# Performance work log

Hardware: AMD Instinct MI355X
Metric: run time of the kernel (lower is better)

Reference implementation:

```python
import jax, jax.numpy as jnp
import numpy as np

B, S, H, DH = 8, 1024, 16, 64
D = H * DH  # d_model = 1024
M_ALPHA = -1e9


def setup_inputs() -> dict:
    key = jax.random.key(0)
    ks = jax.random.split(key, 11)
    scale = 1.0 / np.sqrt(D)
    x = jax.random.normal(ks[0], (B, S, D), dtype=jnp.float32)
    # 0/1 padding mask, shape [B, S, 1] (1 = masked position)
    mask = (jax.random.uniform(ks[1], (B, S, 1)) < 0.25).astype(jnp.float32)
    mk = lambda k: jax.random.normal(k, (D, D), dtype=jnp.float32) * scale
    return {
        "x": x,
        "mask": mask,
        "wq_w": mk(ks[2]), "wq_b": jnp.zeros((D,), jnp.float32),
        "wk_w": mk(ks[3]), "wk_b": jnp.zeros((D,), jnp.float32),
        "wv_w": mk(ks[4]), "wv_b": jnp.zeros((D,), jnp.float32),
        "wo_w": mk(ks[5]), "wo_b": jnp.zeros((D,), jnp.float32),
    }


def _split_heads(t):
    # [B, S, D] -> [B, H, S, DH]
    return t.reshape(B, S, H, DH).transpose(0, 2, 1, 3)


def reference(x, mask, wq_w, wq_b, wk_w, wk_b, wv_w, wv_b, wo_w, wo_b):
    q = _split_heads(x @ wq_w + wq_b)  # [B,H,S,DH]
    k = _split_heads(x @ wk_w + wk_b)
    v = _split_heads(x @ wv_w + wv_b)

    logits = jnp.einsum("bhqd,bhkd->bhqk", q, k) / jnp.sqrt(
        jnp.asarray(DH, jnp.float32))
    qk_values = logits  # pre-mask scaled logits (temperature == 0.0 -> no-op)

    # QK mask path: mask [B,S,1] -> tile to [B,S,S] rows (m[b,i,j] = mask[b,i]),
    # then symmetrize (square) -> mask[b,i] + mask[b,j], clamp at 1.
    m = mask[:, :, 0]                               # [B,S]
    mask_qk = jnp.minimum(1.0, m[:, :, None] + m[:, None, :])  # [B,S,S]
    logits = logits + mask_qk[:, None, :, :] * M_ALPHA

    attn = jax.nn.softmax(logits, axis=-1)          # [B,H,S,S]
    z = jnp.einsum("bhqk,bhkd->bhqd", attn, v)      # [B,H,S,DH]
    z = z.transpose(0, 2, 1, 3).reshape(B, S, D)
    out = z @ wo_w + wo_b
    return (out, attn, qk_values, q, k, v)
```

## Files before the change

kernel.cpp:

```cpp
#include <hip/hip_runtime.h>
#include <hip/hip_bf16.h>
#include <stdint.h>

#define BB 8
#define SS 1024
#define HH 16
#define DHD 64
#define DD 1024

typedef __attribute__((ext_vector_type(8))) short bf16x8;
typedef __attribute__((ext_vector_type(4))) float f32x4;

__device__ __forceinline__ unsigned short f2bf(float f) {
  unsigned u = __builtin_bit_cast(unsigned, f);
  u += 0x7fffu + ((u >> 16) & 1u);
  return (unsigned short)(u >> 16);
}

__device__ __forceinline__ unsigned swz(unsigned a) { return a ^ ((a >> 3) & 0x70u); }

#define GLOAD16(gp, lp)                                                        \
  __builtin_amdgcn_global_load_lds(                                            \
      (const __attribute__((address_space(1))) unsigned int*)(gp),             \
      (__attribute__((address_space(3))) unsigned int*)(lp), 16, 0, 0)

#define MFMA16(a, b, c) __builtin_amdgcn_mfma_f32_16x16x32_bf16(a, b, c, 0, 0, 0)

__global__ __launch_bounds__(256) void cvt_x_kernel(const float* __restrict__ x,
                                                    unsigned short* __restrict__ xb) {
  int i = blockIdx.x * 256 + threadIdx.x;
  float4 v = ((const float4*)x)[i];
  ushort4 o;
  o.x = f2bf(v.x); o.y = f2bf(v.y); o.z = f2bf(v.z); o.w = f2bf(v.w);
  ((ushort4*)xb)[i] = o;
}

__global__ __launch_bounds__(256) void transpose_w_kernel(
    const float* __restrict__ w0, const float* __restrict__ w1,
    const float* __restrict__ w2, const float* __restrict__ w3,
    unsigned short* __restrict__ o0, unsigned short* __restrict__ o1,
    unsigned short* __restrict__ o2, unsigned short* __restrict__ o3) {
  __shared__ float tile[32][33];
  const float* src; unsigned short* dst;
  if (blockIdx.z == 0)      { src = w0; dst = o0; }
  else if (blockIdx.z == 1) { src = w1; dst = o1; }
  else if (blockIdx.z == 2) { src = w2; dst = o2; }
  else                      { src = w3; dst = o3; }
  int n0 = blockIdx.x * 32, k0 = blockIdx.y * 32;
  int tx = threadIdx.x, ty = threadIdx.y;
#pragma unroll
  for (int j = 0; j < 32; j += 8)
    tile[ty + j][tx] = src[(size_t)(k0 + ty + j) * DD + n0 + tx];
  __syncthreads();
#pragma unroll
  for (int j = 0; j < 32; j += 8)
    dst[(size_t)(n0 + ty + j) * DD + k0 + tx] = f2bf(tile[tx][ty + j]);
}

__global__ __launch_bounds__(256) void proj_gemm_kernel(
    const unsigned short* __restrict__ xb,
    const unsigned short* __restrict__ wqt, const unsigned short* __restrict__ wkt,
    const unsigned short* __restrict__ wvt,
    const float* __restrict__ bq, const float* __restrict__ bk, const float* __restrict__ bv,
    float* __restrict__ qo, float* __restrict__ ko, float* __restrict__ vo,
    unsigned short* __restrict__ qb, unsigned short* __restrict__ kbf,
    unsigned short* __restrict__ vt) {
  __shared__ __align__(128) unsigned short smem[2 * 128 * 64];
  unsigned short* As = smem;
  unsigned short* Bs = smem + 128 * 64;
  const int tid = threadIdx.x, lane = tid & 63, w = tid >> 6;
  const int wr = (w >> 1) * 64, wc = (w & 1) * 64;
  const int m0 = blockIdx.x * 128;
  const int mat = blockIdx.y >> 3;
  const int n0 = (blockIdx.y & 7) * 128;
  const unsigned short* Bg = (mat == 0) ? wqt : (mat == 1) ? wkt : wvt;
  const float* bias = (mat == 0) ? bq : (mat == 1) ? bk : bv;

  f32x4 acc[4][4];
  f32x4 z4 = {0.f, 0.f, 0.f, 0.f};
#pragma unroll
  for (int i = 0; i < 4; ++i)
#pragma unroll
    for (int j = 0; j < 4; ++j) acc[i][j] = z4;

  for (int kt = 0; kt < 1024; kt += 64) {
    __syncthreads();
#pragma unroll
    for (int i = 0; i < 4; ++i) {
      unsigned obase = (unsigned)(w * 4096 + i * 1024);
      unsigned a = swz(obase + (unsigned)lane * 16);
      GLOAD16((const char*)xb + ((size_t)(m0 + (int)(a >> 7)) * 1024 + kt) * 2 + (a & 127),
              (char*)As + obase);
      GLOAD16((const char*)Bg + ((size_t)(n0 + (int)(a >> 7)) * 1024 + kt) * 2 + (a & 127),
              (char*)Bs + obase);
    }
    __syncthreads();
#pragma unroll
    for (int ks = 0; ks < 2; ++ks) {
      bf16x8 af[4], bfr[4];
#pragma unroll
      for (int mi = 0; mi < 4; ++mi) {
        unsigned a = (unsigned)((wr + mi * 16 + (lane & 15)) * 128 + ks * 64 + ((lane >> 4) * 16));
        af[mi] = *(const bf16x8*)((const char*)As + swz(a));
      }
#pragma unroll
      for (int ni = 0; ni < 4; ++ni) {
        unsigned a = (unsigned)((wc + ni * 16 + (lane & 15)) * 128 + ks * 64 + ((lane >> 4) * 16));
        bfr[ni] = *(const bf16x8*)((const char*)Bs + swz(a));
      }
#pragma unroll
      for (int mi = 0; mi < 4; ++mi)
#pragma unroll
        for (int ni = 0; ni < 4; ++ni)
          acc[mi][ni] = MFMA16(af[mi], bfr[ni], acc[mi][ni]);
    }
  }

  float* fo = (mat == 0) ? qo : (mat == 1) ? ko : vo;
  __syncthreads();
  unsigned short* T = smem;

#pragma unroll
  for (int mi = 0; mi < 4; ++mi)
#pragma unroll
    for (int ni = 0; ni < 4; ++ni) {
      int col = n0 + wc + ni * 16 + (lane & 15);
      float bs = bias[col];
#pragma unroll
      for (int r = 0; r < 4; ++r) {
        int row = m0 + wr + mi * 16 + ((lane >> 4) << 2) + r;
        float v = acc[mi][ni][r] + bs;
        int b = row >> 10, s = row & 1023, h = col >> 6, dh = col & 63;
        size_t bh = (size_t)(b * HH + h);
        __builtin_nontemporal_store(v, &fo[(bh * SS + s) * DHD + dh]);
        if (mat == 2) {
          int sl = wr + mi * 16 + ((lane >> 4) << 2) + r;
          int dl = wc + ni * 16 + (lane & 15);
          T[dl * 128 + (sl ^ ((dl & 7) << 4))] = f2bf(v);
        } else if (mat == 0) {
          qb[(bh * SS + s) * DHD + dh] = f2bf(v * 0.125f);
        } else {
          kbf[(bh * SS + s) * DHD + dh] = f2bf(v);
        }
      }
    }

  if (mat == 2) {
    __syncthreads();
    int row = tid >> 1;
    int half = tid & 1;
    int colg = n0 + row;
    int h2 = colg >> 6, dh2 = colg & 63;
    int b = m0 >> 10;
    int sg0 = (m0 & 1023) + half * 64;
    unsigned short* dst = vt + (((size_t)(b * HH + h2)) * DHD + dh2) * SS + sg0;
#pragma unroll
    for (int j = 0; j < 8; ++j) {
      int sc = half * 64 + j * 8;
      bf16x8 vv = *(const bf16x8*)&T[row * 128 + (sc ^ ((row & 7) << 4))];
      *(bf16x8*)(dst + j * 8) = vv;
    }
  }
}

__global__ __launch_bounds__(256) void attn_kernel(
    const unsigned short* __restrict__ qb, const unsigned short* __restrict__ kb,
    const unsigned short* __restrict__ vt, const float* __restrict__ mask,
    float* __restrict__ qk_out, float* __restrict__ attn_out,
    unsigned short* __restrict__ zb) {
  __shared__ __align__(128) unsigned short pbuf[4][16 * 64];

  const int tid = threadIdx.x, lane = tid & 63, w = tid >> 6;
  const int fid = blockIdx.x;
  const int bh = fid & 127, qt = fid >> 7;
  const int b = bh >> 4, h = bh & 15;
  const int r0 = qt * 64 + w * 16;
  const int q15 = lane & 15, G = lane >> 4;

  bf16x8 aq[2];
  {
    const unsigned short* p = qb + (size_t)bh * SS * DHD + (size_t)(r0 + q15) * DHD + G * 8;
    aq[0] = *(const bf16x8*)p;
    aq[1] = *(const bf16x8*)(p + 32);
  }
  const float* mrow = mask + (size_t)b * SS;
  const float mq = mrow[r0 + q15];

  const unsigned short* kbase = kb + (size_t)bh * SS * DHD;
  const unsigned short* vbase = vt + (size_t)bh * DHD * SS;
  float* qrow = qk_out + (size_t)bh * SS * SS + (size_t)(r0 + q15) * SS;
  float* arow = attn_out + (size_t)bh * SS * SS + (size_t)(r0 + q15) * SS;

  float m_run = -INFINITY, l_run = 0.f;

  for (int kt = 0; kt < 16; ++kt) {
    int k0 = kt * 64;
    f32x4 sm[4];
#pragma unroll
    for (int ct = 0; ct < 4; ++ct) {
      f32x4 acc = {0.f, 0.f, 0.f, 0.f};
#pragma unroll
      for (int ks = 0; ks < 2; ++ks) {
        bf16x8 bk = *(const bf16x8*)(kbase + (size_t)(k0 + ct * 16 + q15) * 64 + ks * 32 + G * 8);
        acc = MFMA16(bk, aq[ks], acc);
      }
      int c0 = k0 + ct * 16 + G * 4;
      __builtin_nontemporal_store(acc, (f32x4*)(qrow + c0));
      float4 mk4 = *(const float4*)(mrow + c0);
#pragma unroll
      for (int r = 0; r < 4; ++r) {
        float t = fminf(mq + ((const float*)&mk4)[r], 1.f);
        sm[ct][r] = acc[r] + t * (-1.0e9f);
      }
    }
    float mx = sm[0][0];
#pragma unroll
    for (int ct = 0; ct < 4; ++ct)
#pragma unroll
      for (int r = 0; r < 4; ++r) mx = fmaxf(mx, sm[ct][r]);
    mx = fmaxf(mx, __shfl_xor(mx, 16, 64));
    mx = fmaxf(mx, __shfl_xor(mx, 32, 64));
    float m_new = fmaxf(m_run, mx);
    float es = 0.f;
#pragma unroll
    for (int ct = 0; ct < 4; ++ct)
#pragma unroll
      for (int r = 0; r < 4; ++r) es += __expf(sm[ct][r] - m_new);
    es += __shfl_xor(es, 16, 64);
    es += __shfl_xor(es, 32, 64);
    l_run = l_run * __expf(m_run - m_new) + es;
    m_run = m_new;
  }

  const float inv_l = 1.0f / l_run;

  f32x4 zacc[4];
#pragma unroll
  for (int dt = 0; dt < 4; ++dt) zacc[dt] = (f32x4){0.f, 0.f, 0.f, 0.f};

  unsigned short* pw = pbuf[w];
  const unsigned pswz = (unsigned)((q15 & 14) << 3);

  for (int kt = 0; kt < 16; ++kt) {
    int k0 = kt * 64;
#pragma unroll
    for (int ct = 0; ct < 4; ++ct) {
      f32x4 acc = {0.f, 0.f, 0.f, 0.f};
#pragma unroll
      for (int ks = 0; ks < 2; ++ks) {
        bf16x8 bk = *(const bf16x8*)(kbase + (size_t)(k0 + ct * 16 + q15) * 64 + ks * 32 + G * 8);
        acc = MFMA16(bk, aq[ks], acc);
      }
      int c0 = k0 + ct * 16 + G * 4;
      float4 mk4 = *(const float4*)(mrow + c0);
      f32x4 pn;
#pragma unroll
      for (int r = 0; r < 4; ++r) {
        float t = fminf(mq + ((const float*)&mk4)[r], 1.f);
        pn[r] = __expf(acc[r] + t * (-1.0e9f) - m_run) * inv_l;
      }
      __builtin_nontemporal_store(pn, (f32x4*)(arow + c0));
      unsigned u0 = (unsigned)f2bf(pn[0]) | ((unsigned)f2bf(pn[1]) << 16);
      unsigned u1 = (unsigned)f2bf(pn[2]) | ((unsigned)f2bf(pn[3]) << 16);
      uint2 pkd = {u0, u1};
      *(uint2*)((char*)pw + (((unsigned)(q15 * 128 + ct * 32 + G * 8)) ^ pswz)) = pkd;
    }
    bf16x8 pa[2];
#pragma unroll
    for (int ks = 0; ks < 2; ++ks)
      pa[ks] = *(const bf16x8*)((char*)pw + (((unsigned)(q15 * 128 + ks * 64 + G * 16)) ^ pswz));
#pragma unroll
    for (int dt = 0; dt < 4; ++dt) {
#pragma unroll
      for (int ks = 0; ks < 2; ++ks) {
        bf16x8 bv = *(const bf16x8*)(vbase + (size_t)(dt * 16 + q15) * SS + k0 + ks * 32 + G * 8);
        zacc[dt] = MFMA16(pa[ks], bv, zacc[dt]);
      }
    }
  }

#pragma unroll
  for (int dt = 0; dt < 4; ++dt)
#pragma unroll
    for (int r = 0; r < 4; ++r) {
      int srow = r0 + G * 4 + r;
      int dcol = dt * 16 + q15;
      zb[((size_t)b * SS + srow) * DD + h * 64 + dcol] = f2bf(zacc[dt][r]);
    }
}

__global__ __launch_bounds__(256) void out_gemm_kernel(
    const unsigned short* __restrict__ zb, const unsigned short* __restrict__ wot,
    const float* __restrict__ bo, float* __restrict__ outp) {
  __shared__ __align__(128) unsigned short As[128 * 64];
  __shared__ __align__(128) unsigned short Bs[128 * 64];
  const int tid = threadIdx.x, lane = tid & 63, w = tid >> 6;
  const int wr = (w >> 1) * 64, wc = (w & 1) * 64;
  const int m0 = blockIdx.x * 128;
  const int n0 = blockIdx.y * 128;

  f32x4 acc[4][4];
  f32x4 z4 = {0.f, 0.f, 0.f, 0.f};
#pragma unroll
  for (int i = 0; i < 4; ++i)
#pragma unroll
    for (int j = 0; j < 4; ++j) acc[i][j] = z4;

  for (int kt = 0; kt < 1024; kt += 64) {
    __syncthreads();
#pragma unroll
    for (int i = 0; i < 4; ++i) {
      unsigned obase = (unsigned)(w * 4096 + i * 1024);
      unsigned a = swz(obase + (unsigned)lane * 16);
      GLOAD16((const char*)zb + ((size_t)(m0 + (int)(a >> 7)) * 1024 + kt) * 2 + (a & 127),
              (char*)As + obase);
      GLOAD16((const char*)wot + ((size_t)(n0 + (int)(a >> 7)) * 1024 + kt) * 2 + (a & 127),
              (char*)Bs + obase);
    }
    __syncthreads();
#pragma unroll
    for (int ks = 0; ks < 2; ++ks) {
      bf16x8 af[4], bfr[4];
#pragma unroll
      for (int mi = 0; mi < 4; ++mi) {
        unsigned a = (unsigned)((wr + mi * 16 + (lane & 15)) * 128 + ks * 64 + ((lane >> 4) * 16));
        af[mi] = *(const bf16x8*)((const char*)As + swz(a));
      }
#pragma unroll
      for (int ni = 0; ni < 4; ++ni) {
        unsigned a = (unsigned)((wc + ni * 16 + (lane & 15)) * 128 + ks * 64 + ((lane >> 4) * 16));
        bfr[ni] = *(const bf16x8*)((const char*)Bs + swz(a));
      }
#pragma unroll
      for (int mi = 0; mi < 4; ++mi)
#pragma unroll
        for (int ni = 0; ni < 4; ++ni)
          acc[mi][ni] = MFMA16(af[mi], bfr[ni], acc[mi][ni]);
    }
  }
#pragma unroll
  for (int mi = 0; mi < 4; ++mi)
#pragma unroll
    for (int ni = 0; ni < 4; ++ni) {
      int col = n0 + wc + ni * 16 + (lane & 15);
      float bs = bo[col];
#pragma unroll
      for (int r = 0; r < 4; ++r) {
        int row = m0 + wr + mi * 16 + ((lane >> 4) << 2) + r;
        __builtin_nontemporal_store(acc[mi][ni][r] + bs, &outp[(size_t)row * DD + col]);
      }
    }
}

extern "C" void kernel_launch(void* const* d_in, const int* in_sizes, int n_in,
                              void* d_out, int out_size, void* d_ws, size_t ws_size,
                              hipStream_t stream) {
  const float* x    = (const float*)d_in[0];
  const float* mask = (const float*)d_in[1];
  const float* wq_w = (const float*)d_in[2];
  const float* wq_b = (const float*)d_in[3];
  const float* wk_w = (const float*)d_in[4];
  const float* wk_b = (const float*)d_in[5];
  const float* wv_w = (const float*)d_in[6];
  const float* wv_b = (const float*)d_in[7];
  const float* wo_w = (const float*)d_in[8];
  const float* wo_b = (const float*)d_in[9];

  float* outp = (float*)d_out;
  float* attn = outp + (size_t)8388608;
  float* qk   = attn + (size_t)134217728;
  float* qo   = qk + (size_t)134217728;
  float* ko   = qo + (size_t)8388608;
  float* vo   = ko + (size_t)8388608;

  char* ws = (char*)d_ws;
  unsigned short* xb  = (unsigned short*)(ws + 0);
  unsigned short* wqt = (unsigned short*)(ws + 16777216);
  unsigned short* wkt = (unsigned short*)(ws + 18874368);
  unsigned short* wvt = (unsigned short*)(ws + 20971520);
  unsigned short* wot = (unsigned short*)(ws + 23068672);
  unsigned short* qb  = (unsigned short*)(ws + 25165824);
  unsigned short* kb  = (unsigned short*)(ws + 41943040);
  unsigned short* vt  = (unsigned short*)(ws + 58720256);
  unsigned short* zb  = (unsigned short*)(ws + 75497472);

  cvt_x_kernel<<<8192, 256, 0, stream>>>(x, xb);
  transpose_w_kernel<<<dim3(32, 32, 4), dim3(32, 8), 0, stream>>>(
      wq_w, wk_w, wv_w, wo_w, wqt, wkt, wvt, wot);
  proj_gemm_kernel<<<dim3(64, 24), 256, 0, stream>>>(
      xb, wqt, wkt, wvt, wq_b, wk_b, wv_b, qo, ko, vo, qb, kb, vt);
  attn_kernel<<<2048, 256, 0, stream>>>(qb, kb, vt, mask, qk, attn, zb);
  out_gemm_kernel<<<dim3(64, 8), 256, 0, stream>>>(zb, wot, wo_b, outp);
}
```

Baseline: 561.5 us.

## Stage K and V tiles in LDS with double-buffered async global loads

The attention kernel now loads 64x64 K and V^T tiles cooperatively into swizzled, double-buffered shared memory using global_load_lds, and prefetches the next tile while computing on the current one. Before this, each wave read K and V straight from global memory with per-lane 16-byte loads, which duplicated traffic across the four waves. The change adds block-wide barriers every iteration and 32KB of extra LDS, which may lower occupancy. The kernel is likely dominated by the large fp32 qk and attn stores, so the benefit may be limited.

```diff
diff --git a/kernel.cpp b/kernel.cpp
--- a/kernel.cpp
+++ b/kernel.cpp
@@ -168,6 +168,8 @@
     const unsigned short* __restrict__ vt, const float* __restrict__ mask,
     float* __restrict__ qk_out, float* __restrict__ attn_out,
     unsigned short* __restrict__ zb) {
+  __shared__ __align__(128) unsigned short kbuf[2][64 * 64];
+  __shared__ __align__(128) unsigned short vbuf[2][64 * 64];
   __shared__ __align__(128) unsigned short pbuf[4][16 * 64];
 
   const int tid = threadIdx.x, lane = tid & 63, w = tid >> 6;
@@ -186,22 +188,38 @@
   const float* mrow = mask + (size_t)b * SS;
   const float mq = mrow[r0 + q15];
 
-  const unsigned short* kbase = kb + (size_t)bh * SS * DHD;
-  const unsigned short* vbase = vt + (size_t)bh * DHD * SS;
+  const char* kbase = (const char*)(kb + (size_t)bh * SS * DHD);
+  const char* vbase = (const char*)(vt + (size_t)bh * DHD * SS);
   float* qrow = qk_out + (size_t)bh * SS * SS + (size_t)(r0 + q15) * SS;
   float* arow = attn_out + (size_t)bh * SS * SS + (size_t)(r0 + q15) * SS;
 
+  const unsigned obase0 = (unsigned)(w * 2048);
+  const unsigned a0 = swz(obase0 + (unsigned)lane * 16);
+  const unsigned obase1 = obase0 + 1024;
+  const unsigned a1 = swz(obase1 + (unsigned)lane * 16);
+
   float m_run = -INFINITY, l_run = 0.f;
 
+  GLOAD16(kbase + a0, (char*)kbuf[0] + obase0);
+  GLOAD16(kbase + a1, (char*)kbuf[0] + obase1);
+  __syncthreads();
+  int cur = 0;
   for (int kt = 0; kt < 16; ++kt) {
     int k0 = kt * 64;
+    if (kt < 15) {
+      const char* kb_n = kbase + (size_t)(k0 + 64) * 128;
+      GLOAD16(kb_n + a0, (char*)kbuf[cur ^ 1] + obase0);
+      GLOAD16(kb_n + a1, (char*)kbuf[cur ^ 1] + obase1);
+    }
+    const char* kc = (const char*)kbuf[cur];
     f32x4 sm[4];
 #pragma unroll
     for (int ct = 0; ct < 4; ++ct) {
       f32x4 acc = {0.f, 0.f, 0.f, 0.f};
 #pragma unroll
       for (int ks = 0; ks < 2; ++ks) {
-        bf16x8 bk = *(const bf16x8*)(kbase + (size_t)(k0 + ct * 16 + q15) * 64 + ks * 32 + G * 8);
+        unsigned a = (unsigned)((ct * 16 + q15) * 128 + ks * 64 + G * 16);
+        bf16x8 bk = *(const bf16x8*)(kc + swz(a));
         acc = MFMA16(bk, aq[ks], acc);
       }
       int c0 = k0 + ct * 16 + G * 4;
@@ -230,6 +248,8 @@
     es += __shfl_xor(es, 32, 64);
     l_run = l_run * __expf(m_run - m_new) + es;
     m_run = m_new;
+    __syncthreads();
+    cur ^= 1;
   }
 
   const float inv_l = 1.0f / l_run;
@@ -241,14 +261,33 @@
   unsigned short* pw = pbuf[w];
   const unsigned pswz = (unsigned)((q15 & 14) << 3);
 
+  GLOAD16(kbase + a0, (char*)kbuf[0] + obase0);
+  GLOAD16(kbase + a1, (char*)kbuf[0] + obase1);
+  GLOAD16(vbase + (size_t)(a0 >> 7) * (SS * 2) + (a0 & 127), (char*)vbuf[0] + obase0);
+  GLOAD16(vbase + (size_t)(a1 >> 7) * (SS * 2) + (a1 & 127), (char*)vbuf[0] + obase1);
+  __syncthreads();
+  cur = 0;
   for (int kt = 0; kt < 16; ++kt) {
     int k0 = kt * 64;
+    if (kt < 15) {
+      int kn = k0 + 64;
+      const char* kb_n = kbase + (size_t)kn * 128;
+      GLOAD16(kb_n + a0, (char*)kbuf[cur ^ 1] + obase0);
+      GLOAD16(kb_n + a1, (char*)kbuf[cur ^ 1] + obase1);
+      GLOAD16(vbase + (size_t)(a0 >> 7) * (SS * 2) + (size_t)kn * 2 + (a0 & 127),
+              (char*)vbuf[cur ^ 1] + obase0);
+      GLOAD16(vbase + (size_t)(a1 >> 7) * (SS * 2) + (size_t)kn * 2 + (a1 & 127),
+              (char*)vbuf[cur ^ 1] + obase1);
+    }
+    const char* kc = (const char*)kbuf[cur];
+    const char* vc = (const char*)vbuf[cur];
 #pragma unroll
     for (int ct = 0; ct < 4; ++ct) {
       f32x4 acc = {0.f, 0.f, 0.f, 0.f};
 #pragma unroll
       for (int ks = 0; ks < 2; ++ks) {
-        bf16x8 bk = *(const bf16x8*)(kbase + (size_t)(k0 + ct * 16 + q15) * 64 + ks * 32 + G * 8);
+        unsigned a = (unsigned)((ct * 16 + q15) * 128 + ks * 64 + G * 16);
+        bf16x8 bk = *(const bf16x8*)(kc + swz(a));
         acc = MFMA16(bk, aq[ks], acc);
       }
       int c0 = k0 + ct * 16 + G * 4;
@@ -273,10 +312,13 @@
     for (int dt = 0; dt < 4; ++dt) {
 #pragma unroll
       for (int ks = 0; ks < 2; ++ks) {
-        bf16x8 bv = *(const bf16x8*)(vbase + (size_t)(dt * 16 + q15) * SS + k0 + ks * 32 + G * 8);
+        unsigned av = (unsigned)((dt * 16 + q15) * 128 + ks * 64 + G * 16);
+        bf16x8 bv = *(const bf16x8*)(vc + swz(av));
         zacc[dt] = MFMA16(pa[ks], bv, zacc[dt]);
       }
     }
+    __syncthreads();
+    cur ^= 1;
   }
 
 #pragma unroll
```

Result: faster. 538.4 us (-4.1%).
